# Optimization experiments

Measured on AMD Instinct MI355X. Metric: run time of the kernel, lower is better.

Reference implementation:

```python
import jax, jax.numpy as jnp
import numpy as np

NB = 31      # num_bands
PD = 64      # processing_dim


def _conv(x, w, b, groups, pad):
    # x: NCHW, w: OIHW (I = in_channels/groups)
    y = jax.lax.conv_general_dilated(
        x, w, window_strides=(1, 1), padding=pad,
        feature_group_count=groups,
        dimension_numbers=('NCHW', 'OIHW', 'NCHW'))
    return y + b[None, :, None, None]


def _gelu(z):
    # torch.nn.GELU() default is exact (erf-based)
    return jax.nn.gelu(z, approximate=False)


def setup_inputs() -> dict:
    key = jax.random.key(0)
    ks = jax.random.split(key, 11)
    s = 0.05
    inp = {
        'x':   jax.random.normal(ks[0], (2, NB, 192, 192), dtype=jnp.float32),
        # 31 independent band processors, stacked as grouped-conv weights (groups=31)
        'W1':  jax.random.normal(ks[1], (NB * PD, 1, 3, 3), dtype=jnp.float32) * s,
        'b1':  jax.random.normal(ks[2], (NB * PD,), dtype=jnp.float32) * s,
        'W2':  jax.random.normal(ks[3], (NB * PD, PD, 3, 3), dtype=jnp.float32) * s,
        'b2':  jax.random.normal(ks[4], (NB * PD,), dtype=jnp.float32) * s,
        'W3':  jax.random.normal(ks[5], (NB, PD, 1, 1), dtype=jnp.float32) * s,
        'b3':  jax.random.normal(ks[6], (NB,), dtype=jnp.float32) * s,
        # cross-band fusion 1x1 convs
        'Wf1': jax.random.normal(ks[7], (NB * 2, NB, 1, 1), dtype=jnp.float32) * s,
        'bf1': jax.random.normal(ks[8], (NB * 2,), dtype=jnp.float32) * s,
        'Wf2': jax.random.normal(ks[9], (NB, NB * 2, 1, 1), dtype=jnp.float32) * s,
        'bf2': jax.random.normal(ks[10], (NB,), dtype=jnp.float32) * s,
    }
    return inp


def reference(x, W1, b1, W2, b2, W3, b3, Wf1, bf1, Wf2, bf2):
    P3 = [(1, 1), (1, 1)]
    P1 = [(0, 0), (0, 0)]
    # per-band 3-layer stacks expressed as grouped convs (groups = num_bands)
    h = _gelu(_conv(x, W1, b1, NB, P3))           # [B, 31*64, H, W]
    h = _gelu(_conv(h, W2, b2, NB, P3))           # [B, 31*64, H, W]
    processed = _conv(h, W3, b3, NB, P1)          # [B, 31, H, W]
    # cross-band fusion
    f = _gelu(_conv(processed, Wf1, bf1, 1, P1))  # [B, 62, H, W]
    fused = _conv(f, Wf2, bf2, 1, P1)             # [B, 31, H, W]
    return x + fused
```

## Files before the change

kernel.cpp:

```cpp
#include <hip/hip_runtime.h>
#include <hip/hip_bf16.h>

#define NB 31
#define PD 64

typedef __attribute__((ext_vector_type(8))) short short8;
typedef __attribute__((ext_vector_type(16))) float f32x16;
typedef __attribute__((ext_vector_type(8))) int int8v;

__device__ __forceinline__ float gelu_f(float x) {
    float y = x * x;
    float p = __builtin_fmaf(y, __builtin_fmaf(y, 0.0042294f, -0.056913f), 0.395442f);
    float phi;
    asm("v_fma_f32 %0, %1, %2, 0.5 clamp" : "=v"(phi) : "v"(x), "v"(p));
    return x * phi;
}

__device__ __forceinline__ unsigned int cvt_pk_bf16(float lo, float hi) {
    unsigned int r;
    asm("v_cvt_pk_bf16_f32 %0, %1, %2" : "=v"(r) : "v"(lo), "v"(hi));
    return r;
}

__device__ __forceinline__ unsigned int pk_fp8(float a, float b) {
    return (unsigned int)__builtin_amdgcn_cvt_pk_fp8_f32(a, b, 0, false);
}

__device__ __forceinline__ int8v mk8(uint4 a, uint4 b) {
    int8v r;
    r[0] = a.x; r[1] = a.y; r[2] = a.z; r[3] = a.w;
    r[4] = b.x; r[5] = b.y; r[6] = b.z; r[7] = b.w;
    return r;
}

__global__ void prep_w2(const float* __restrict__ W2, unsigned char* __restrict__ W2s) {
    int e = blockIdx.x * 256 + threadIdx.x;
    const int TOT = NB * 2 * 9 * 64;
    if (e >= TOT) return;
    int lane = e & 63;
    int tap  = (e >> 6) % 9;
    int gh   = e / (9 * 64);
    int g = gh >> 1, oh = gh & 1;
    int col = lane & 31, hi = lane >> 5;
    const float* wp = W2 + ((size_t)(g * 64 + oh * 32 + col) * 64 + hi * 32) * 9 + tap;
    unsigned int d[8];
#pragma unroll
    for (int i = 0; i < 8; ++i) {
        float f0 = wp[(4 * i + 0) * 9];
        float f1 = wp[(4 * i + 1) * 9];
        float f2 = wp[(4 * i + 2) * 9];
        float f3 = wp[(4 * i + 3) * 9];
        d[i] = pk_fp8(f0, f1) | (pk_fp8(f2, f3) << 16);
    }
    uint4 q0, q1;
    q0.x = d[0]; q0.y = d[2]; q0.z = d[4]; q0.w = d[6];
    q1.x = d[1]; q1.y = d[3]; q1.z = d[5]; q1.w = d[7];
    uint4* op = (uint4*)W2s + (size_t)e * 2;
    op[0] = q0; op[1] = q1;
}

__global__ __launch_bounds__(512, 5) void band_kernel(
    const float* __restrict__ x, const float* __restrict__ W1, const float* __restrict__ b1,
    const float* __restrict__ b2, const float* __restrict__ W3, const float* __restrict__ b3,
    const unsigned char* __restrict__ W2s, float* __restrict__ out)
{
    __shared__ float xs[20 * 20];
    __shared__ uint4 h1s[352 * 5];
    __shared__ float outs[2 * 256];

    const int tid = threadIdx.x;
    const int tx = blockIdx.x % 12, ty = blockIdx.x / 12;
    const int g = blockIdx.y, n = blockIdx.z;
    const int x0 = tx * 16, y0 = ty * 16;

    const int lane = tid & 63;
    const int wid  = tid >> 6;
    const int w4   = wid & 3;
    const int oh   = wid >> 2;
    const int hi   = lane >> 5;
    const int col  = lane & 31;

    const float* xg = x + (size_t)(n * NB + g) * 192 * 192;
    if (tid < 400) {
        int r = tid / 20, c = tid - r * 20;
        int gy = y0 + r - 2, gx = x0 + c - 2;
        float v = 0.f;
        if (gy >= 0 && gy < 192 && gx >= 0 && gx < 192) v = xg[gy * 192 + gx];
        xs[tid] = v;
    }

    short8 a1;
    {
        const float* wp = W1 + (size_t)(g * 64 + oh * 32 + col) * 9;
        uint4 bw = {0u, 0u, 0u, 0u};
        if (hi == 0) {
            bw.x = cvt_pk_bf16(wp[0], wp[1]);
            bw.y = cvt_pk_bf16(wp[2], wp[3]);
            bw.z = cvt_pk_bf16(wp[4], wp[5]);
            bw.w = cvt_pk_bf16(wp[6], wp[7]);
        } else {
            bw.x = cvt_pk_bf16(wp[8], b1[g * 64 + oh * 32 + col]);
        }
        a1 = __builtin_bit_cast(short8, bw);
    }
    __syncthreads();

    char* h1c = (char*)h1s;
#pragma unroll
    for (int it = 0; it < 3; ++it) {
        const int t = w4 + 4 * it;
        if (t < 11) {
            const int posr = t * 32 + col;
            const int pos  = posr < 324 ? posr : 323;
            int py = pos / 18, px = pos - py * 18;
            int gy = y0 + py - 1, gx = x0 + px - 1;
            unsigned int msk = (gy >= 0 && gy < 192 && gx >= 0 && gx < 192) ? 0xFFFFFFFFu : 0u;

            uint4 bw = {0u, 0u, 0u, 0u};
            if (hi == 0) {
                float xv[8];
#pragma unroll
                for (int j2 = 0; j2 < 8; ++j2)
                    xv[j2] = xs[(py + j2 / 3) * 20 + px + (j2 % 3)];
                bw.x = cvt_pk_bf16(xv[0], xv[1]);
                bw.y = cvt_pk_bf16(xv[2], xv[3]);
                bw.z = cvt_pk_bf16(xv[4], xv[5]);
                bw.w = cvt_pk_bf16(xv[6], xv[7]);
            } else {
                bw.x = cvt_pk_bf16(xs[(py + 2) * 20 + px + 2], 1.0f);
            }
            short8 bfrag = __builtin_bit_cast(short8, bw);

            f32x16 z = {};
            f32x16 c0 = __builtin_amdgcn_mfma_f32_32x32x16_bf16(a1, bfrag, z, 0, 0, 0);

            uint4 st;
            {
                float u0 = gelu_f(c0[0]),  u1 = gelu_f(c0[1]);
                float u2 = gelu_f(c0[2]),  u3 = gelu_f(c0[3]);
                st.x = (pk_fp8(u0, u1) | (pk_fp8(u2, u3) << 16)) & msk;
            }
            {
                float u0 = gelu_f(c0[4]),  u1 = gelu_f(c0[5]);
                float u2 = gelu_f(c0[6]),  u3 = gelu_f(c0[7]);
                st.y = (pk_fp8(u0, u1) | (pk_fp8(u2, u3) << 16)) & msk;
            }
            {
                float u0 = gelu_f(c0[8]),  u1 = gelu_f(c0[9]);
                float u2 = gelu_f(c0[10]), u3 = gelu_f(c0[11]);
                st.z = (pk_fp8(u0, u1) | (pk_fp8(u2, u3) << 16)) & msk;
            }
            {
                float u0 = gelu_f(c0[12]), u1 = gelu_f(c0[13]);
                float u2 = gelu_f(c0[14]), u3 = gelu_f(c0[15]);
                st.w = (pk_fp8(u0, u1) | (pk_fp8(u2, u3) << 16)) & msk;
            }
            *(uint4*)(h1c + posr * 80 + (oh << 5) + (hi << 4)) = st;
        }
    }
    __syncthreads();

    const int lhalf = (lane >> 4) & 1;
    const int pxl   = lane & 15;
    const int base0 = (4 * w4 + lhalf) * 18 + pxl;

    const int gh = g * 2 + oh;
    const uint4* ap = (const uint4*)W2s + (size_t)gh * 9 * 128 + lane * 2;

    f32x16 acc0, acc1;
    {
        const float* bp = b2 + g * 64 + oh * 32 + 4 * hi;
#pragma unroll
        for (int s = 0; s < 4; ++s) {
            float4 q = *(const float4*)(bp + 8 * s);
            acc0[4 * s + 0] = q.x; acc0[4 * s + 1] = q.y;
            acc0[4 * s + 2] = q.z; acc0[4 * s + 3] = q.w;
            acc1[4 * s + 0] = q.x; acc1[4 * s + 1] = q.y;
            acc1[4 * s + 2] = q.z; acc1[4 * s + 3] = q.w;
        }
    }

    uint4 Aq[3][2];
    Aq[0][0] = ap[0];   Aq[0][1] = ap[1];
    Aq[1][0] = ap[128]; Aq[1][1] = ap[129];

#pragma unroll
    for (int tap = 0; tap < 9; ++tap) {
        if (tap + 2 < 9) {
            Aq[(tap + 2) % 3][0] = ap[(tap + 2) * 128];
            Aq[(tap + 2) % 3][1] = ap[(tap + 2) * 128 + 1];
        }
        const int D = (tap / 3) * 18 + (tap % 3);
        const int p0 = base0 + D;
        const int p1 = p0 + 36;
        const char* r0 = h1c + p0 * 80 + (hi << 5);
        const char* r1 = h1c + p1 * 80 + (hi << 5);
        uint4 b0a = *(const uint4*)(r0);
        uint4 b0b = *(const uint4*)(r0 + 16);
        uint4 b1a = *(const uint4*)(r1);
        uint4 b1b = *(const uint4*)(r1 + 16);
        int8v A = mk8(Aq[tap % 3][0], Aq[tap % 3][1]);
        acc0 = __builtin_amdgcn_mfma_scale_f32_32x32x64_f8f6f4(
                   A, mk8(b0a, b0b), acc0, 0, 0, 0, 0x7F7F7F7F, 0, 0x7F7F7F7F);
        acc1 = __builtin_amdgcn_mfma_scale_f32_32x32x64_f8f6f4(
                   A, mk8(b1a, b1b), acc1, 0, 0, 0, 0x7F7F7F7F, 0, 0x7F7F7F7F);
    }

    float pa = 0.f, pb = 0.f;
    {
        const float* wp3 = W3 + g * 64 + oh * 32 + 4 * hi;
#pragma unroll
        for (int s = 0; s < 4; ++s) {
            float4 qa = *(const float4*)(wp3 + 8 * s);
            pa = __builtin_fmaf(qa.x, gelu_f(acc0[4 * s + 0]), pa);
            pa = __builtin_fmaf(qa.y, gelu_f(acc0[4 * s + 1]), pa);
            pa = __builtin_fmaf(qa.z, gelu_f(acc0[4 * s + 2]), pa);
            pa = __builtin_fmaf(qa.w, gelu_f(acc0[4 * s + 3]), pa);
            pb = __builtin_fmaf(qa.x, gelu_f(acc1[4 * s + 0]), pb);
            pb = __builtin_fmaf(qa.y, gelu_f(acc1[4 * s + 1]), pb);
            pb = __builtin_fmaf(qa.z, gelu_f(acc1[4 * s + 2]), pb);
            pb = __builtin_fmaf(qa.w, gelu_f(acc1[4 * s + 3]), pb);
        }
    }
    pa += __shfl_xor(pa, 32);
    pb += __shfl_xor(pb, 32);
    if (lane < 32) {
        outs[oh * 256 + w4 * 64 + lane]      = pa;
        outs[oh * 256 + w4 * 64 + 32 + lane] = pb;
    }
    __syncthreads();

    if (tid < 256) {
        float v = outs[tid] + outs[256 + tid] + b3[g];
        int py = 4 * (tid >> 6) + 2 * ((tid >> 5) & 1) + ((tid >> 4) & 1);
        int px = tid & 15;
        out[((size_t)(n * NB + g) * 192 + y0 + py) * 192 + x0 + px] = v;
    }
}

__global__ __launch_bounds__(512) void fuse_kernel(
    const float* __restrict__ x,
    const float* __restrict__ Wf1, const float* __restrict__ bf1,
    const float* __restrict__ Wf2, const float* __restrict__ bf2,
    float* __restrict__ out)
{
    __shared__ float part[256 * 33];
    const int tid  = threadIdx.x;
    const int half = __builtin_amdgcn_readfirstlane(tid >> 8);
    const int pixl = tid & 255;
    int p = blockIdx.x * 256 + pixl;
    int nn = p / 36864, pix = p - nn * 36864;
    float* basep = out + (size_t)nn * NB * 36864 + pix;
    const float* xb = x + (size_t)nn * NB * 36864 + pix;

    float v[31];
#pragma unroll
    for (int c = 0; c < 31; ++c) v[c] = basep[(size_t)c * 36864];

    float fused[31];
#pragma unroll
    for (int c = 0; c < 31; ++c) fused[c] = 0.f;

    for (int jj = 0; jj < 31; ++jj) {
        int j = half * 31 + jj;
        float a = bf1[j];
#pragma unroll
        for (int c = 0; c < 31; ++c) a = __builtin_fmaf(Wf1[j * 31 + c], v[c], a);
        float fj = gelu_f(a);
#pragma unroll
        for (int c = 0; c < 31; ++c) fused[c] = __builtin_fmaf(Wf2[c * 62 + j], fj, fused[c]);
    }

    if (half == 1) {
#pragma unroll
        for (int c = 0; c < 31; ++c) part[pixl * 33 + c] = fused[c];
    }
    __syncthreads();
    if (half == 0) {
#pragma unroll
        for (int c = 0; c < 31; ++c)
            basep[(size_t)c * 36864] =
                xb[(size_t)c * 36864] + fused[c] + part[pixl * 33 + c] + bf2[c];
    }
}

extern "C" void kernel_launch(void* const* d_in, const int* in_sizes, int n_in,
                              void* d_out, int out_size, void* d_ws, size_t ws_size,
                              hipStream_t stream) {
    const float* x   = (const float*)d_in[0];
    const float* W1  = (const float*)d_in[1];
    const float* b1  = (const float*)d_in[2];
    const float* W2  = (const float*)d_in[3];
    const float* b2  = (const float*)d_in[4];
    const float* W3  = (const float*)d_in[5];
    const float* b3  = (const float*)d_in[6];
    const float* Wf1 = (const float*)d_in[7];
    const float* bf1 = (const float*)d_in[8];
    const float* Wf2 = (const float*)d_in[9];
    const float* bf2 = (const float*)d_in[10];
    float* out = (float*)d_out;
    unsigned char* W2s = (unsigned char*)d_ws;

    const int TOT = NB * 2 * 9 * 64;
    hipLaunchKernelGGL(prep_w2, dim3((TOT + 255) / 256), dim3(256), 0, stream, W2, W2s);
    hipLaunchKernelGGL(band_kernel, dim3(144, NB, 2), dim3(512), 0, stream,
                       x, W1, b1, b2, W3, b3, W2s, out);
    hipLaunchKernelGGL(fuse_kernel, dim3(288), dim3(512), 0, stream,
                       x, Wf1, bf1, Wf2, bf2, out);
}
```

Baseline: 172.6 us.

## Process two 16x16 tiles per block, overlapping second conv1 with first conv2

Each band_kernel block now covers a 32x16 region as two 16x16 tiles. The first conv layer for the second tile is interleaved with the conv2 MFMA taps of the first tile, and the x halo load is shared between the two tiles. This is meant to hide conv1/GELU latency behind conv2 matrix work and to halve the block count. The cost is twice the h1 LDS buffer and occupancy lowered from 5 to 4 blocks per CU, and the W2 prefetch ring is replaced by direct loads inside each tap group.

```diff
diff --git a/kernel.cpp b/kernel.cpp
--- a/kernel.cpp
+++ b/kernel.cpp
@@ -59,19 +59,19 @@
     op[0] = q0; op[1] = q1;
 }
 
-__global__ __launch_bounds__(512, 5) void band_kernel(
+__global__ __launch_bounds__(512, 4) void band_kernel(
     const float* __restrict__ x, const float* __restrict__ W1, const float* __restrict__ b1,
     const float* __restrict__ b2, const float* __restrict__ W3, const float* __restrict__ b3,
     const unsigned char* __restrict__ W2s, float* __restrict__ out)
 {
-    __shared__ float xs[20 * 20];
-    __shared__ uint4 h1s[352 * 5];
+    __shared__ float xs[20 * 36];
+    __shared__ uint4 h1s[704 * 5];
     __shared__ float outs[2 * 256];
 
     const int tid = threadIdx.x;
-    const int tx = blockIdx.x % 12, ty = blockIdx.x / 12;
+    const int txp = blockIdx.x % 6, ty = blockIdx.x / 6;
     const int g = blockIdx.y, n = blockIdx.z;
-    const int x0 = tx * 16, y0 = ty * 16;
+    const int x0c = txp * 32, y0 = ty * 16;
 
     const int lane = tid & 63;
     const int wid  = tid >> 6;
@@ -81,12 +81,12 @@
     const int col  = lane & 31;
 
     const float* xg = x + (size_t)(n * NB + g) * 192 * 192;
-    if (tid < 400) {
-        int r = tid / 20, c = tid - r * 20;
-        int gy = y0 + r - 2, gx = x0 + c - 2;
+    for (int i = tid; i < 720; i += 512) {
+        int r = i / 36, c = i - r * 36;
+        int gy = y0 + r - 2, gx = x0c + c - 2;
         float v = 0.f;
         if (gy >= 0 && gy < 192 && gx >= 0 && gx < 192) v = xg[gy * 192 + gx];
-        xs[tid] = v;
+        xs[i] = v;
     }
 
     short8 a1;
@@ -106,14 +106,19 @@
     __syncthreads();
 
     char* h1c = (char*)h1s;
-#pragma unroll
-    for (int it = 0; it < 3; ++it) {
+    const int lhalf = (lane >> 4) & 1;
+    const int pxl   = lane & 15;
+    const int base0 = (4 * w4 + lhalf) * 18 + pxl;
+    const int gh = g * 2 + oh;
+    const uint4* ap = (const uint4*)W2s + (size_t)gh * 9 * 128 + lane * 2;
+
+    auto conv1_iter = [&](int T, int it) {
         const int t = w4 + 4 * it;
         if (t < 11) {
             const int posr = t * 32 + col;
             const int pos  = posr < 324 ? posr : 323;
             int py = pos / 18, px = pos - py * 18;
-            int gy = y0 + py - 1, gx = x0 + px - 1;
+            int gy = y0 + py - 1, gx = x0c + T * 16 + px - 1;
             unsigned int msk = (gy >= 0 && gy < 192 && gx >= 0 && gx < 192) ? 0xFFFFFFFFu : 0u;
 
             uint4 bw = {0u, 0u, 0u, 0u};
@@ -121,13 +126,13 @@
                 float xv[8];
 #pragma unroll
                 for (int j2 = 0; j2 < 8; ++j2)
-                    xv[j2] = xs[(py + j2 / 3) * 20 + px + (j2 % 3)];
+                    xv[j2] = xs[(py + j2 / 3) * 36 + T * 16 + px + (j2 % 3)];
                 bw.x = cvt_pk_bf16(xv[0], xv[1]);
                 bw.y = cvt_pk_bf16(xv[2], xv[3]);
                 bw.z = cvt_pk_bf16(xv[4], xv[5]);
                 bw.w = cvt_pk_bf16(xv[6], xv[7]);
             } else {
-                bw.x = cvt_pk_bf16(xs[(py + 2) * 20 + px + 2], 1.0f);
+                bw.x = cvt_pk_bf16(xs[(py + 2) * 36 + T * 16 + px + 2], 1.0f);
             }
             short8 bfrag = __builtin_bit_cast(short8, bw);
 
@@ -155,87 +160,96 @@
                 float u2 = gelu_f(c0[14]), u3 = gelu_f(c0[15]);
                 st.w = (pk_fp8(u0, u1) | (pk_fp8(u2, u3) << 16)) & msk;
             }
-            *(uint4*)(h1c + posr * 80 + (oh << 5) + (hi << 4)) = st;
-        }
-    }
-    __syncthreads();
-
-    const int lhalf = (lane >> 4) & 1;
-    const int pxl   = lane & 15;
-    const int base0 = (4 * w4 + lhalf) * 18 + pxl;
-
-    const int gh = g * 2 + oh;
-    const uint4* ap = (const uint4*)W2s + (size_t)gh * 9 * 128 + lane * 2;
-
-    f32x16 acc0, acc1;
-    {
+            *(uint4*)(h1c + T * 28160 + posr * 80 + (oh << 5) + (hi << 4)) = st;
+        }
+    };
+
+    auto acc_init = [&](f32x16& A0v, f32x16& A1v) {
         const float* bp = b2 + g * 64 + oh * 32 + 4 * hi;
 #pragma unroll
         for (int s = 0; s < 4; ++s) {
             float4 q = *(const float4*)(bp + 8 * s);
-            acc0[4 * s + 0] = q.x; acc0[4 * s + 1] = q.y;
-            acc0[4 * s + 2] = q.z; acc0[4 * s + 3] = q.w;
-            acc1[4 * s + 0] = q.x; acc1[4 * s + 1] = q.y;
-            acc1[4 * s + 2] = q.z; acc1[4 * s + 3] = q.w;
-        }
-    }
-
-    uint4 Aq[3][2];
-    Aq[0][0] = ap[0];   Aq[0][1] = ap[1];
-    Aq[1][0] = ap[128]; Aq[1][1] = ap[129];
-
-#pragma unroll
-    for (int tap = 0; tap < 9; ++tap) {
-        if (tap + 2 < 9) {
-            Aq[(tap + 2) % 3][0] = ap[(tap + 2) * 128];
-            Aq[(tap + 2) % 3][1] = ap[(tap + 2) * 128 + 1];
-        }
-        const int D = (tap / 3) * 18 + (tap % 3);
-        const int p0 = base0 + D;
-        const int p1 = p0 + 36;
-        const char* r0 = h1c + p0 * 80 + (hi << 5);
-        const char* r1 = h1c + p1 * 80 + (hi << 5);
-        uint4 b0a = *(const uint4*)(r0);
-        uint4 b0b = *(const uint4*)(r0 + 16);
-        uint4 b1a = *(const uint4*)(r1);
-        uint4 b1b = *(const uint4*)(r1 + 16);
-        int8v A = mk8(Aq[tap % 3][0], Aq[tap % 3][1]);
-        acc0 = __builtin_amdgcn_mfma_scale_f32_32x32x64_f8f6f4(
-                   A, mk8(b0a, b0b), acc0, 0, 0, 0, 0x7F7F7F7F, 0, 0x7F7F7F7F);
-        acc1 = __builtin_amdgcn_mfma_scale_f32_32x32x64_f8f6f4(
-                   A, mk8(b1a, b1b), acc1, 0, 0, 0, 0x7F7F7F7F, 0, 0x7F7F7F7F);
-    }
-
-    float pa = 0.f, pb = 0.f;
-    {
+            A0v[4 * s + 0] = q.x; A0v[4 * s + 1] = q.y;
+            A0v[4 * s + 2] = q.z; A0v[4 * s + 3] = q.w;
+            A1v[4 * s + 0] = q.x; A1v[4 * s + 1] = q.y;
+            A1v[4 * s + 2] = q.z; A1v[4 * s + 3] = q.w;
+        }
+    };
+
+    auto conv2_taps = [&](int T, int tap0, f32x16& A0v, f32x16& A1v) {
+#pragma unroll
+        for (int tt = 0; tt < 3; ++tt) {
+            const int tap = tap0 + tt;
+            const int D = (tap / 3) * 18 + (tap % 3);
+            const int p0 = base0 + D;
+            const int p1 = p0 + 36;
+            const char* r0 = h1c + T * 28160 + p0 * 80 + (hi << 5);
+            const char* r1 = h1c + T * 28160 + p1 * 80 + (hi << 5);
+            uint4 b0a = *(const uint4*)(r0);
+            uint4 b0b = *(const uint4*)(r0 + 16);
+            uint4 b1a = *(const uint4*)(r1);
+            uint4 b1b = *(const uint4*)(r1 + 16);
+            uint4 al = ap[tap * 128], ah = ap[tap * 128 + 1];
+            int8v A = mk8(al, ah);
+            A0v = __builtin_amdgcn_mfma_scale_f32_32x32x64_f8f6f4(
+                      A, mk8(b0a, b0b), A0v, 0, 0, 0, 0x7F7F7F7F, 0, 0x7F7F7F7F);
+            A1v = __builtin_amdgcn_mfma_scale_f32_32x32x64_f8f6f4(
+                      A, mk8(b1a, b1b), A1v, 0, 0, 0, 0x7F7F7F7F, 0, 0x7F7F7F7F);
+        }
+    };
+
+    auto epilogue = [&](f32x16& A0v, f32x16& A1v) {
+        float pa = 0.f, pb = 0.f;
         const float* wp3 = W3 + g * 64 + oh * 32 + 4 * hi;
 #pragma unroll
         for (int s = 0; s < 4; ++s) {
             float4 qa = *(const float4*)(wp3 + 8 * s);
-            pa = __builtin_fmaf(qa.x, gelu_f(acc0[4 * s + 0]), pa);
-            pa = __builtin_fmaf(qa.y, gelu_f(acc0[4 * s + 1]), pa);
-            pa = __builtin_fmaf(qa.z, gelu_f(acc0[4 * s + 2]), pa);
-            pa = __builtin_fmaf(qa.w, gelu_f(acc0[4 * s + 3]), pa);
-            pb = __builtin_fmaf(qa.x, gelu_f(acc1[4 * s + 0]), pb);
-            pb = __builtin_fmaf(qa.y, gelu_f(acc1[4 * s + 1]), pb);
-            pb = __builtin_fmaf(qa.z, gelu_f(acc1[4 * s + 2]), pb);
-            pb = __builtin_fmaf(qa.w, gelu_f(acc1[4 * s + 3]), pb);
-        }
-    }
-    pa += __shfl_xor(pa, 32);
-    pb += __shfl_xor(pb, 32);
-    if (lane < 32) {
-        outs[oh * 256 + w4 * 64 + lane]      = pa;
-        outs[oh * 256 + w4 * 64 + 32 + lane] = pb;
-    }
-    __syncthreads();
-
-    if (tid < 256) {
-        float v = outs[tid] + outs[256 + tid] + b3[g];
-        int py = 4 * (tid >> 6) + 2 * ((tid >> 5) & 1) + ((tid >> 4) & 1);
-        int px = tid & 15;
-        out[((size_t)(n * NB + g) * 192 + y0 + py) * 192 + x0 + px] = v;
-    }
+            pa = __builtin_fmaf(qa.x, gelu_f(A0v[4 * s + 0]), pa);
+            pa = __builtin_fmaf(qa.y, gelu_f(A0v[4 * s + 1]), pa);
+            pa = __builtin_fmaf(qa.z, gelu_f(A0v[4 * s + 2]), pa);
+            pa = __builtin_fmaf(qa.w, gelu_f(A0v[4 * s + 3]), pa);
+            pb = __builtin_fmaf(qa.x, gelu_f(A1v[4 * s + 0]), pb);
+            pb = __builtin_fmaf(qa.y, gelu_f(A1v[4 * s + 1]), pb);
+            pb = __builtin_fmaf(qa.z, gelu_f(A1v[4 * s + 2]), pb);
+            pb = __builtin_fmaf(qa.w, gelu_f(A1v[4 * s + 3]), pb);
+        }
+        pa += __shfl_xor(pa, 32);
+        pb += __shfl_xor(pb, 32);
+        if (lane < 32) {
+            outs[oh * 256 + w4 * 64 + lane]      = pa;
+            outs[oh * 256 + w4 * 64 + 32 + lane] = pb;
+        }
+    };
+
+    auto outwrite = [&](int T) {
+        if (tid < 256) {
+            float v = outs[tid] + outs[256 + tid] + b3[g];
+            int py_ = 4 * (tid >> 6) + 2 * ((tid >> 5) & 1) + ((tid >> 4) & 1);
+            int px_ = tid & 15;
+            out[((size_t)(n * NB + g) * 192 + y0 + py_) * 192 + x0c + T * 16 + px_] = v;
+        }
+    };
+
+    conv1_iter(0, 0); conv1_iter(0, 1); conv1_iter(0, 2);
+    __syncthreads();
+
+    f32x16 acc0, acc1;
+    acc_init(acc0, acc1);
+    conv1_iter(1, 0); conv2_taps(0, 0, acc0, acc1);
+    conv1_iter(1, 1); conv2_taps(0, 3, acc0, acc1);
+    conv1_iter(1, 2); conv2_taps(0, 6, acc0, acc1);
+    epilogue(acc0, acc1);
+    __syncthreads();
+    outwrite(0);
+    __syncthreads();
+
+    acc_init(acc0, acc1);
+    conv2_taps(1, 0, acc0, acc1);
+    conv2_taps(1, 3, acc0, acc1);
+    conv2_taps(1, 6, acc0, acc1);
+    epilogue(acc0, acc1);
+    __syncthreads();
+    outwrite(1);
 }
 
 __global__ __launch_bounds__(512) void fuse_kernel(
@@ -303,7 +317,7 @@
 
     const int TOT = NB * 2 * 9 * 64;
     hipLaunchKernelGGL(prep_w2, dim3((TOT + 255) / 256), dim3(256), 0, stream, W2, W2s);
-    hipLaunchKernelGGL(band_kernel, dim3(144, NB, 2), dim3(512), 0, stream,
+    hipLaunchKernelGGL(band_kernel, dim3(72, NB, 2), dim3(512), 0, stream,
                        x, W1, b1, b2, W3, b3, W2s, out);
     hipLaunchKernelGGL(fuse_kernel, dim3(288), dim3(512), 0, stream,
                        x, Wf1, bf1, Wf2, bf2, out);
```

New measurement: 157.8 us. 8.5% less time.
